# Kernel optimization log

Hardware: AMD Instinct MI355X
Metric: run time of the kernel (lower is better)

Reference implementation:

```python
import jax, jax.numpy as jnp
import numpy as np
from jax import lax

# GlobalSeed with a standard Mamba2 (SSD) core.
# C=64 feature channels, G=8 token dim, d_inner=16, d_state=16, nheads=2, headdim=8, d_conv=3.
C_FEAT, G, D_INNER, D_STATE, NHEADS, HEADDIM, D_CONV = 64, 8, 16, 16, 2, 8, 3
CONV_DIM = D_INNER + 2 * D_STATE  # 48
D_IN_PROJ = 2 * D_INNER + 2 * D_STATE + NHEADS  # 66


def setup_inputs() -> dict:
    key = jax.random.key(0)
    ks = jax.random.split(key, 16)
    B, H, W = 16, 128, 128
    s = 0.02
    return {
        "x": jax.random.normal(ks[0], (B, C_FEAT, H, W), jnp.float32),
        "tok_w": s * jax.random.normal(ks[1], (G, C_FEAT), jnp.float32),
        "tok_b": jnp.zeros((G,), jnp.float32),
        "detok_w": s * jax.random.normal(ks[2], (C_FEAT, G), jnp.float32),
        "detok_b": jnp.zeros((C_FEAT,), jnp.float32),
        "in_proj_w": s * jax.random.normal(ks[3], (D_IN_PROJ, G), jnp.float32),
        "in_proj_b": jnp.zeros((D_IN_PROJ,), jnp.float32),
        "conv_w": s * jax.random.normal(ks[4], (CONV_DIM, D_CONV), jnp.float32),
        "conv_b": jnp.zeros((CONV_DIM,), jnp.float32),
        "A_log": jnp.log(jnp.arange(1, NHEADS + 1, dtype=jnp.float32)),
        "D": jnp.ones((NHEADS,), jnp.float32),
        "dt_bias": 0.1 * jax.random.normal(ks[5], (NHEADS,), jnp.float32),
        "norm_w": jnp.ones((D_INNER,), jnp.float32),
        "out_w": s * jax.random.normal(ks[6], (G, D_INNER), jnp.float32),
        "out_b": jnp.zeros((G,), jnp.float32),
    }


def _mamba2(gt, in_proj_w, in_proj_b, conv_w, conv_b, A_log, D, dt_bias, norm_w, out_w, out_b):
    # gt: (B, L, G) tokens
    B, L, _ = gt.shape
    zxbcdt = gt @ in_proj_w.T + in_proj_b  # (B, L, 66)
    z = zxbcdt[..., :D_INNER]
    xBC = zxbcdt[..., D_INNER:D_INNER + CONV_DIM]
    dt = zxbcdt[..., D_INNER + CONV_DIM:]  # (B, L, nheads)
    # depthwise causal conv1d over L
    xBC = lax.conv_general_dilated(
        xBC.transpose(0, 2, 1), conv_w[:, None, :], (1,), [(D_CONV - 1, 0)],
        feature_group_count=CONV_DIM).transpose(0, 2, 1) + conv_b
    xBC = jax.nn.silu(xBC)
    xr = xBC[..., :D_INNER].reshape(B, L, NHEADS, HEADDIM)
    Bm = xBC[..., D_INNER:D_INNER + D_STATE]   # (B, L, N)
    Cm = xBC[..., D_INNER + D_STATE:]          # (B, L, N)
    dt = jax.nn.softplus(dt + dt_bias)          # (B, L, H)
    dec = jnp.exp(dt * (-jnp.exp(A_log)))       # (B, L, H)

    def step(h, inp):
        xt, Bt, Ct, dtt, dct = inp  # (B,H,P) (B,N) (B,N) (B,H) (B,H)
        h = dct[:, :, None, None] * h + (dtt[:, :, None] * xt)[..., None] * Bt[:, None, None, :]
        y = jnp.einsum('bhpn,bn->bhp', h, Ct)
        return h, y

    h0 = jnp.zeros((B, NHEADS, HEADDIM, D_STATE), gt.dtype)
    xs = (xr.transpose(1, 0, 2, 3), Bm.transpose(1, 0, 2), Cm.transpose(1, 0, 2),
          dt.transpose(1, 0, 2), dec.transpose(1, 0, 2))
    _, ys = lax.scan(step, h0, xs)  # (L, B, H, P)
    y = ys.transpose(1, 0, 2, 3) + D[None, None, :, None] * xr
    y = y.reshape(B, L, D_INNER)
    y = y * jax.nn.silu(z)  # gated
    y = y * lax.rsqrt(jnp.mean(y * y, axis=-1, keepdims=True) + 1e-5) * norm_w  # RMSNormGated
    return y @ out_w.T + out_b  # (B, L, G)


def reference(x, tok_w, tok_b, detok_w, detok_b, in_proj_w, in_proj_b, conv_w, conv_b,
              A_log, D, dt_bias, norm_w, out_w, out_b):
    B, C, H, W = x.shape
    L = H * W
    g = jnp.einsum('bchw,gc->bghw', x, tok_w) + tok_b[None, :, None, None]
    gt = g.reshape(B, G, L).transpose(0, 2, 1)  # (B, L, G)
    gt = _mamba2(gt, in_proj_w, in_proj_b, conv_w, conv_b, A_log, D, dt_bias, norm_w, out_w, out_b) + gt
    g2 = gt.transpose(0, 2, 1).reshape(B, G, H, W)
    return x + jnp.einsum('bghw,cg->bchw', g2, detok_w) + detok_b[None, :, None, None]
```

## Files before the change

kernel.cpp:

```cpp
#include <hip/hip_runtime.h>
#include <math.h>

#define NB 16
#define CF 64
#define LL 16384
#define GG 8
#define NH 2
#define CHN 64
#define NCH 256
#define NGRP 16

static constexpr size_t OFF_GT = 0;
static constexpr size_t OFF_C  = OFF_GT + (size_t)NB*LL*GG;
static constexpr size_t OFF_YL = OFF_C  + (size_t)NB*LL*16;
static constexpr size_t OFF_CA = OFF_YL + (size_t)NB*LL*16;
static constexpr size_t OFF_U2 = OFF_CA + (size_t)NB*LL*NH;
static constexpr size_t OFF_AC = OFF_U2 + (size_t)NB*NCH*256;
static constexpr size_t OFF_PH = OFF_AC + (size_t)NB*NCH*NH;
static constexpr size_t OFF_CP = OFF_PH + (size_t)NB*NCH*256;
static constexpr size_t OFF_UG = OFF_CP + (size_t)NB*NCH*NH;
static constexpr size_t OFF_AG = OFF_UG + (size_t)NB*NGRP*256;
static constexpr size_t OFF_GH = OFF_AG + (size_t)NB*NGRP*NH;
static constexpr size_t OFF_G2 = OFF_GH + (size_t)NB*NGRP*256;
static constexpr size_t WS_FLOATS = OFF_G2 + (size_t)NB*LL*GG;

typedef float f32x4 __attribute__((ext_vector_type(4)));
typedef short bf16x8 __attribute__((ext_vector_type(8)));

__device__ __forceinline__ float siluf(float v){ return v / (1.f + __expf(-v)); }
__device__ __forceinline__ float softplusf(float v){ return v > 20.f ? v : log1pf(__expf(v)); }

__device__ __forceinline__ unsigned short f2bf(float f){
    unsigned int u = __float_as_uint(f);
    u += 0x7fffu + ((u >> 16) & 1u);
    return (unsigned short)(u >> 16);
}
__device__ __forceinline__ float bf2f(unsigned short s){
    return __uint_as_float(((unsigned int)s) << 16);
}

__device__ __forceinline__ void load8(float* d, const float* p){
    float4 a = ((const float4*)p)[0];
    float4 b = ((const float4*)p)[1];
    d[0]=a.x; d[1]=a.y; d[2]=a.z; d[3]=a.w;
    d[4]=b.x; d[5]=b.y; d[6]=b.z; d[7]=b.w;
}
__device__ __forceinline__ void load16(float* d, const float* p){
    load8(d, p); load8(d+8, p+8);
}

__global__ __launch_bounds__(64) void k1a_tok(
    const float* __restrict__ x, const float* __restrict__ tok_w,
    const float* __restrict__ tok_b, float* __restrict__ gtw)
{
    __shared__ float s_tok[GG*CF];
    int tid = threadIdx.x;
    int b  = blockIdx.x >> 6;
    int ck = blockIdx.x & 63;
    int l0 = (ck << 8) + (tid << 2);
    for (int i = tid; i < GG*CF; i += 64) s_tok[i] = tok_w[i];
    __syncthreads();
    float acc[4][GG];
    #pragma unroll
    for (int r = 0; r < 4; ++r)
        #pragma unroll
        for (int g = 0; g < GG; ++g) acc[r][g] = tok_b[g];
    const float* xb = x + (size_t)b*CF*LL + l0;
    #pragma unroll 8
    for (int c = 0; c < CF; ++c) {
        float4 xv = *(const float4*)(xb + (size_t)c*LL);
        float xa[4] = {xv.x, xv.y, xv.z, xv.w};
        #pragma unroll
        for (int g = 0; g < GG; ++g) {
            float w = s_tok[g*CF + c];
            #pragma unroll
            for (int r = 0; r < 4; ++r) acc[r][g] = fmaf(xa[r], w, acc[r][g]);
        }
    }
    float* gp = gtw + ((size_t)b*LL + l0)*GG;
    #pragma unroll
    for (int r = 0; r < 4; ++r) {
        ((float4*)gp)[r*2+0] = make_float4(acc[r][0],acc[r][1],acc[r][2],acc[r][3]);
        ((float4*)gp)[r*2+1] = make_float4(acc[r][4],acc[r][5],acc[r][6],acc[r][7]);
    }
}

__global__ __launch_bounds__(256, 3) void k2_ssd(
    const float* __restrict__ gtw,
    const float* __restrict__ ipw, const float* __restrict__ ipb,
    const float* __restrict__ cw, const float* __restrict__ cb,
    const float* __restrict__ A_log, const float* __restrict__ dt_bias,
    const float* __restrict__ Dv,
    float* __restrict__ cmw, float* __restrict__ ylw, float* __restrict__ caw,
    float* __restrict__ U2w, float* __restrict__ Acw)
{
    __shared__ __align__(16) unsigned short Cbf[64*40];
    __shared__ __align__(16) unsigned short Bbf[64*40];
    __shared__ __align__(16) unsigned short XTbf[16*72];
    __shared__ __align__(16) unsigned short BTbf[16*72];
    __shared__ __align__(16) unsigned short WXbf[16*72];
    __shared__ __align__(16) unsigned short M0[64*72];
    __shared__ __align__(16) unsigned short M1[64*72];
    __shared__ __align__(16) float s_xf[64*20];
    __shared__ float s_dt[64][2], s_nda[64][2], s_la[64][2], s_w[64][2];
    __shared__ float s_ipw[48*8], s_ipb2[48], s_cw2[144], s_cb2[48], s_wdt[16];

    int tid = threadIdx.x;
    int b = blockIdx.x >> 8, c = blockIdx.x & 255;
    for (int i = tid; i < 384; i += 256) s_ipw[i] = ipw[128 + i];
    if (tid < 48) { s_ipb2[tid] = ipb[16 + tid]; s_cb2[tid] = cb[tid]; }
    else if (tid >= 64 && tid < 208) s_cw2[tid - 64] = cw[tid - 64];
    else if (tid >= 224 && tid < 240) s_wdt[tid - 224] = ipw[512 + (tid - 224)];
    __syncthreads();

    float a0e = __expf(A_log[0]), a1e = __expf(A_log[1]);
    float dtb0 = dt_bias[0], dtb1 = dt_bias[1];
    float bdt0 = ipb[64], bdt1 = ipb[65];
    float D0 = Dv[0], D1 = Dv[1];

    {
        int r = tid >> 2, sub = tid & 3;
        int l = c*CHN + r;
        size_t gb = ((size_t)b*LL + l)*GG;
        float g0[8], g1[8], g2v[8];
        #pragma unroll
        for (int g = 0; g < 8; ++g) { g1[g] = 0.f; g2v[g] = 0.f; }
        load8(g0, gtw + gb);
        if (l >= 1) load8(g1, gtw + gb - GG);
        if (l >= 2) load8(g2v, gtw + gb - 2*GG);
        #pragma unroll
        for (int k = 0; k < 12; ++k) {
            int ch = sub*12 + k;
            float bia = s_ipb2[ch];
            float tA = bia, tB = bia, tC = bia;
            #pragma unroll
            for (int g = 0; g < 8; ++g) {
                float wv = s_ipw[ch*8+g];
                tA = fmaf(g0[g],  wv, tA);
                tB = fmaf(g1[g],  wv, tB);
                tC = fmaf(g2v[g], wv, tC);
            }
            if (l < 1) tB = 0.f;
            if (l < 2) tC = 0.f;
            float a = s_cb2[ch];
            a = fmaf(tC, s_cw2[ch*3+0], a);
            a = fmaf(tB, s_cw2[ch*3+1], a);
            a = fmaf(tA, s_cw2[ch*3+2], a);
            float v = siluf(a);
            if (ch < 16) {
                s_xf[r*20 + ch] = v;
                XTbf[ch*72 + r] = f2bf(v);
            } else if (ch < 32) {
                int n = ch - 16;
                unsigned short bv = f2bf(v);
                Bbf[r*40 + n] = bv;
                BTbf[n*72 + r] = bv;
            } else {
                Cbf[r*40 + (ch - 32)] = f2bf(v);
            }
        }
        unsigned int* cz = (unsigned int*)&Cbf[r*40 + 16];
        unsigned int* bz = (unsigned int*)&Bbf[r*40 + 16];
        cz[sub*2+0] = 0u; cz[sub*2+1] = 0u;
        bz[sub*2+0] = 0u; bz[sub*2+1] = 0u;
        if (sub == 0) {
            float d0 = bdt0, d1 = bdt1;
            #pragma unroll
            for (int g = 0; g < 8; ++g) {
                d0 = fmaf(g0[g], s_wdt[g],   d0);
                d1 = fmaf(g0[g], s_wdt[8+g], d1);
            }
            float dt0 = softplusf(d0 + dtb0), dt1 = softplusf(d1 + dtb1);
            s_dt[r][0] = dt0; s_dt[r][1] = dt1;
            s_nda[r][0] = -dt0*a0e; s_nda[r][1] = -dt1*a1e;
        }
    }
    __syncthreads();

    if (tid < 64) {
        int rr = tid;
        float v0 = s_nda[rr][0], v1 = s_nda[rr][1];
        #pragma unroll
        for (int off = 1; off < 64; off <<= 1) {
            float t0 = __shfl_up(v0, off);
            float t1 = __shfl_up(v1, off);
            if (rr >= off) { v0 += t0; v1 += t1; }
        }
        s_la[rr][0] = v0; s_la[rr][1] = v1;
        *(float2*)(caw + ((size_t)b*LL + c*CHN + rr)*2) =
            make_float2(__expf(v0), __expf(v1));
        float f0 = __shfl(v0, 63), f1 = __shfl(v1, 63);
        s_w[rr][0] = __expf(f0 - v0) * s_dt[rr][0];
        s_w[rr][1] = __expf(f1 - v1) * s_dt[rr][1];
        if (rr == 63)
            *(float2*)(Acw + ((size_t)b*NCH + c)*2) = make_float2(__expf(f0), __expf(f1));
    }
    {
        int rr = tid >> 2, q = tid & 3;
        float4 cv;
        cv.x = bf2f(Cbf[rr*40 + q*4 + 0]);
        cv.y = bf2f(Cbf[rr*40 + q*4 + 1]);
        cv.z = bf2f(Cbf[rr*40 + q*4 + 2]);
        cv.w = bf2f(Cbf[rr*40 + q*4 + 3]);
        ((float4*)(cmw + ((size_t)b*LL + c*CHN + rr)*16))[q] = cv;
    }
    __syncthreads();

    int lane = tid & 63, wv = tid >> 6;
    int ar = lane & 15;
    int kb = lane >> 4;
    int trow = wv*16 + kb*4;

    {
        bf16x8 aC = *(const bf16x8*)&Cbf[(wv*16 + ar)*40 + kb*8];
        float lr0 = s_la[wv*16][0], lr1 = s_la[wv*16][1];
        float ef0[4], ef1[4];
        #pragma unroll
        for (int rg = 0; rg < 4; ++rg) {
            ef0[rg] = __expf(s_la[trow+rg][0] - lr0);
            ef1[rg] = __expf(s_la[trow+rg][1] - lr1);
        }
        for (int ss = 0; ss < 4; ++ss) {
            int s = ss*16 + ar;
            if (ss > wv) {
                #pragma unroll
                for (int rg = 0; rg < 4; ++rg) {
                    M0[(trow+rg)*72 + s] = 0;
                    M1[(trow+rg)*72 + s] = 0;
                }
                continue;
            }
            f32x4 g = {0.f, 0.f, 0.f, 0.f};
            bf16x8 bB = *(const bf16x8*)&Bbf[(ss*16 + ar)*40 + kb*8];
            g = __builtin_amdgcn_mfma_f32_16x16x32_bf16(aC, bB, g, 0, 0, 0);
            float ec0 = __expf(lr0 - s_la[s][0]) * s_dt[s][0];
            float ec1 = __expf(lr1 - s_la[s][1]) * s_dt[s][1];
            #pragma unroll
            for (int rg = 0; rg < 4; ++rg) {
                int t = trow + rg;
                float gv = g[rg];
                float m0 = (s <= t) ? ef0[rg]*ec0*gv : 0.f;
                float m1 = (s <= t) ? ef1[rg]*ec1*gv : 0.f;
                M0[t*72 + s] = f2bf(m0);
                M1[t*72 + s] = f2bf(m1);
            }
        }
    }
    #pragma unroll
    for (int i = 0; i < 4; ++i) {
        int e = tid + 256*i;
        int s = e >> 4, pp = e & 15;
        WXbf[pp*72 + s] = f2bf(s_w[s][pp>>3] * s_xf[s*20 + pp]);
    }
    __syncthreads();

    float* yb = (float*)Cbf;
    {
        int p = ar;
        #pragma unroll
        for (int h = 0; h < 2; ++h) {
            const unsigned short* Mh = h ? M1 : M0;
            f32x4 acc = {0.f, 0.f, 0.f, 0.f};
            #pragma unroll
            for (int kk = 0; kk < 2; ++kk) {
                bf16x8 am = *(const bf16x8*)&Mh[(wv*16 + ar)*72 + kk*32 + kb*8];
                bf16x8 bx = {0,0,0,0,0,0,0,0};
                if (p < 8) bx = *(const bf16x8*)&XTbf[(h*8 + p)*72 + kk*32 + kb*8];
                acc = __builtin_amdgcn_mfma_f32_16x16x32_bf16(am, bx, acc, 0, 0, 0);
            }
            if (p < 8) {
                float Dh = h ? D1 : D0;
                #pragma unroll
                for (int rg = 0; rg < 4; ++rg) {
                    int t = trow + rg;
                    yb[t*20 + h*8 + p] = fmaf(Dh, s_xf[t*20 + h*8 + p], acc[rg]);
                }
            }
        }
    }
    if (wv == 0) {
        f32x4 acc = {0.f, 0.f, 0.f, 0.f};
        #pragma unroll
        for (int kk = 0; kk < 2; ++kk) {
            bf16x8 aw = *(const bf16x8*)&WXbf[ar*72 + kk*32 + kb*8];
            bf16x8 bb = *(const bf16x8*)&BTbf[ar*72 + kk*32 + kb*8];
            acc = __builtin_amdgcn_mfma_f32_16x16x32_bf16(aw, bb, acc, 0, 0, 0);
        }
        #pragma unroll
        for (int rg = 0; rg < 4; ++rg) {
            int pr = kb*4 + rg;
            U2w[(((size_t)b*NCH + c) << 8) + pr*16 + ar] = acc[rg];
        }
    }
    __syncthreads();

    {
        int rr = tid >> 2, q = tid & 3;
        ((float4*)(ylw + ((size_t)b*LL + c*CHN + rr)*16))[q] = *(float4*)&yb[rr*20 + q*4];
    }
}

__global__ void k4c1(const float* __restrict__ U2w, const float* __restrict__ Acw,
                     float* __restrict__ phw, float* __restrict__ cpw,
                     float* __restrict__ Ugw, float* __restrict__ Agw)
{
    int b = blockIdx.x >> 4, grp = blockIdx.x & 15;
    int e = threadIdx.x, he = e >> 7;
    size_t base = (size_t)b*NCH + grp*16;
    float u[16], A[16];
    #pragma unroll
    for (int j = 0; j < 16; ++j) u[j] = U2w[((base + j) << 8) + e];
    #pragma unroll
    for (int j = 0; j < 16; ++j) A[j] = Acw[(base + j)*2 + he];
    float h = 0.f, cp = 1.f;
    #pragma unroll
    for (int j = 0; j < 16; ++j) {
        phw[((base + j) << 8) + e] = h;
        if ((e & 127) == 0) cpw[(base + j)*2 + he] = cp;
        h = fmaf(A[j], h, u[j]);
        cp *= A[j];
    }
    Ugw[(((size_t)b*NGRP + grp) << 8) + e] = h;
    if ((e & 127) == 0) Agw[((size_t)b*NGRP + grp)*2 + he] = cp;
}

__global__ void k4c2(const float* __restrict__ Ugw, const float* __restrict__ Agw,
                     float* __restrict__ ghw)
{
    int b = blockIdx.x, e = threadIdx.x, he = e >> 7;
    float u[NGRP], ag[NGRP];
    #pragma unroll
    for (int g = 0; g < NGRP; ++g) {
        u[g]  = Ugw[(((size_t)b*NGRP + g) << 8) + e];
        ag[g] = Agw[((size_t)b*NGRP + g)*2 + he];
    }
    float h = 0.f;
    #pragma unroll
    for (int g = 0; g < NGRP; ++g) {
        ghw[(((size_t)b*NGRP + g) << 8) + e] = h;
        h = fmaf(ag[g], h, u[g]);
    }
}

__global__ __launch_bounds__(256, 4) void k5a_epi(
    const float* __restrict__ gtw, const float* __restrict__ cmw,
    const float* __restrict__ ylw, const float* __restrict__ caw,
    const float* __restrict__ phw, const float* __restrict__ cpw,
    const float* __restrict__ ghw,
    const float* __restrict__ ipw, const float* __restrict__ ipb,
    const float* __restrict__ norm_w,
    const float* __restrict__ out_w, const float* __restrict__ out_b,
    float* __restrict__ g2w)
{
    __shared__ float s_hin[4][256];
    __shared__ float s_zw[16*GG], s_ow[GG*16];
    int tid = threadIdx.x;
    int b  = blockIdx.x >> 6;
    int ck = blockIdx.x & 63;
    int grpg = ck >> 2;
    float gh = ghw[(((size_t)b*NGRP + grpg) << 8) + tid];
    #pragma unroll
    for (int k = 0; k < 4; ++k) {
        int chn = ck*4 + k;
        float cpv = cpw[((size_t)b*NCH + chn)*2 + (tid >> 7)];
        s_hin[k][tid] = fmaf(cpv, gh, phw[(((size_t)b*NCH + chn) << 8) + tid]);
    }
    if (tid < 128) s_zw[tid] = ipw[tid];
    else s_ow[tid-128] = out_w[tid-128];
    __syncthreads();
    size_t pb = (size_t)b*LL + (ck<<8) + tid;
    int sub = tid >> 6;
    float gv[8]; load8(gv, gtw + pb*GG);
    float Cv[16], ylv[16];
    load16(Cv,  cmw + pb*16);
    load16(ylv, ylw + pb*16);
    float2 ca = *(const float2*)(caw + pb*2);
    float vv[16], ss = 0.f;
    #pragma unroll
    for (int hp = 0; hp < 16; ++hp) {
        float dot = 0.f;
        #pragma unroll
        for (int nn = 0; nn < 16; ++nn)
            dot = fmaf(Cv[nn], s_hin[sub][(hp>>3)*128 + (hp&7)*16 + nn], dot);
        float zz = ipb[hp];
        #pragma unroll
        for (int g = 0; g < GG; ++g) zz = fmaf(gv[g], s_zw[hp*GG+g], zz);
        float y = fmaf((hp>>3) ? ca.y : ca.x, dot, ylv[hp]);
        float w = y * siluf(zz);
        vv[hp] = w; ss = fmaf(w, w, ss);
    }
    float rn = rsqrtf(ss*(1.f/16.f) + 1e-5f);
    float o[8];
    #pragma unroll
    for (int g = 0; g < GG; ++g) o[g] = out_b[g] + gv[g];
    #pragma unroll
    for (int hp = 0; hp < 16; ++hp) {
        float wv = vv[hp] * rn * norm_w[hp];
        #pragma unroll
        for (int g = 0; g < GG; ++g) o[g] = fmaf(wv, s_ow[g*16+hp], o[g]);
    }
    float* gp = g2w + pb*GG;
    ((float4*)gp)[0] = make_float4(o[0],o[1],o[2],o[3]);
    ((float4*)gp)[1] = make_float4(o[4],o[5],o[6],o[7]);
}

__global__ __launch_bounds__(64) void k5b_detok(
    const float* __restrict__ x, const float* __restrict__ g2w,
    const float* __restrict__ dkw, const float* __restrict__ dkb,
    float* __restrict__ outp)
{
    __shared__ float s_dw[CF*GG];
    __shared__ float s_db[CF];
    int tid = threadIdx.x;
    int b  = blockIdx.x >> 6;
    int ck = blockIdx.x & 63;
    int l0 = (ck << 8) + (tid << 2);
    for (int i = tid; i < CF*GG; i += 64) s_dw[i] = dkw[i];
    s_db[tid] = dkb[tid];
    __syncthreads();
    float g2v[4][8];
    const float* gp = g2w + ((size_t)b*LL + l0)*GG;
    #pragma unroll
    for (int r = 0; r < 4; ++r) load8(g2v[r], gp + r*GG);
    const float* xb = x + (size_t)b*CF*LL + l0;
    float* ob = outp + (size_t)b*CF*LL + l0;
    #pragma unroll 4
    for (int c = 0; c < CF; ++c) {
        float4 xv = *(const float4*)(xb + (size_t)c*LL);
        float bias = s_db[c];
        float oa[4] = {xv.x+bias, xv.y+bias, xv.z+bias, xv.w+bias};
        #pragma unroll
        for (int g = 0; g < GG; ++g) {
            float w = s_dw[c*GG+g];
            #pragma unroll
            for (int r = 0; r < 4; ++r) oa[r] = fmaf(g2v[r][g], w, oa[r]);
        }
        *(float4*)(ob + (size_t)c*LL) = make_float4(oa[0],oa[1],oa[2],oa[3]);
    }
}

extern "C" void kernel_launch(void* const* d_in, const int* in_sizes, int n_in,
                              void* d_out, int out_size, void* d_ws, size_t ws_size,
                              hipStream_t stream) {
    const float* x       = (const float*)d_in[0];
    const float* tok_w   = (const float*)d_in[1];
    const float* tok_b   = (const float*)d_in[2];
    const float* detok_w = (const float*)d_in[3];
    const float* detok_b = (const float*)d_in[4];
    const float* ipw     = (const float*)d_in[5];
    const float* ipb     = (const float*)d_in[6];
    const float* cw      = (const float*)d_in[7];
    const float* cb      = (const float*)d_in[8];
    const float* A_log   = (const float*)d_in[9];
    const float* Dv      = (const float*)d_in[10];
    const float* dt_bias = (const float*)d_in[11];
    const float* norm_w  = (const float*)d_in[12];
    const float* out_w   = (const float*)d_in[13];
    const float* out_b   = (const float*)d_in[14];
    float* ws = (float*)d_ws;
    float* outp = (float*)d_out;

    if (ws_size < WS_FLOATS * sizeof(float)) return;

    k1a_tok<<<NB*64, 64, 0, stream>>>(x, tok_w, tok_b, ws+OFF_GT);
    k2_ssd<<<NB*NCH, 256, 0, stream>>>(ws+OFF_GT, ipw, ipb, cw, cb,
        A_log, dt_bias, Dv, ws+OFF_C, ws+OFF_YL, ws+OFF_CA, ws+OFF_U2, ws+OFF_AC);
    k4c1<<<NB*NGRP, 256, 0, stream>>>(ws+OFF_U2, ws+OFF_AC,
        ws+OFF_PH, ws+OFF_CP, ws+OFF_UG, ws+OFF_AG);
    k4c2<<<NB, 256, 0, stream>>>(ws+OFF_UG, ws+OFF_AG, ws+OFF_GH);
    k5a_epi<<<NB*64, 256, 0, stream>>>(ws+OFF_GT, ws+OFF_C, ws+OFF_YL, ws+OFF_CA,
        ws+OFF_PH, ws+OFF_CP, ws+OFF_GH, ipw, ipb, norm_w, out_w, out_b, ws+OFF_G2);
    k5b_detok<<<NB*64, 64, 0, stream>>>(x, ws+OFF_G2, detok_w, detok_b, outp);
}
```

Before: 129.8 us.

## Split SSD into state-only pass and recompute-fused intra-chunk plus epilogue kernel

The first SSD pass now computes only the chunk-end state contributions (x and B channels). The intra-chunk output, the inter-chunk state correction (done as an extra MFMA with decay-scaled C) and the gated RMSNorm/out-proj epilogue are fused into a second per-chunk kernel that recomputes the conv/projections. This removes the C, y_local and cumulative-decay intermediates written to and re-read from global memory. In exchange the in_proj/conv/scan work is done twice, and the cross-chunk state term now goes through bf16 MFMA instead of fp32 FMAs.

```diff
diff --git a/kernel.cpp b/kernel.cpp
--- a/kernel.cpp
+++ b/kernel.cpp
@@ -11,10 +11,7 @@
 #define NGRP 16
 
 static constexpr size_t OFF_GT = 0;
-static constexpr size_t OFF_C  = OFF_GT + (size_t)NB*LL*GG;
-static constexpr size_t OFF_YL = OFF_C  + (size_t)NB*LL*16;
-static constexpr size_t OFF_CA = OFF_YL + (size_t)NB*LL*16;
-static constexpr size_t OFF_U2 = OFF_CA + (size_t)NB*LL*NH;
+static constexpr size_t OFF_U2 = OFF_GT + (size_t)NB*LL*GG;
 static constexpr size_t OFF_AC = OFF_U2 + (size_t)NB*NCH*256;
 static constexpr size_t OFF_PH = OFF_AC + (size_t)NB*NCH*NH;
 static constexpr size_t OFF_CP = OFF_PH + (size_t)NB*NCH*256;
@@ -38,15 +35,15 @@
 __device__ __forceinline__ float bf2f(unsigned short s){
     return __uint_as_float(((unsigned int)s) << 16);
 }
+__device__ __forceinline__ unsigned int pack2bf(float lo, float hi){
+    return (unsigned int)f2bf(lo) | ((unsigned int)f2bf(hi) << 16);
+}
 
 __device__ __forceinline__ void load8(float* d, const float* p){
     float4 a = ((const float4*)p)[0];
     float4 b = ((const float4*)p)[1];
     d[0]=a.x; d[1]=a.y; d[2]=a.z; d[3]=a.w;
     d[4]=b.x; d[5]=b.y; d[6]=b.z; d[7]=b.w;
-}
-__device__ __forceinline__ void load16(float* d, const float* p){
-    load8(d, p); load8(d+8, p+8);
 }
 
 __global__ __launch_bounds__(64) void k1a_tok(
@@ -85,38 +82,30 @@
     }
 }
 
-__global__ __launch_bounds__(256, 3) void k2_ssd(
+__global__ __launch_bounds__(256) void k2a_state(
     const float* __restrict__ gtw,
     const float* __restrict__ ipw, const float* __restrict__ ipb,
     const float* __restrict__ cw, const float* __restrict__ cb,
     const float* __restrict__ A_log, const float* __restrict__ dt_bias,
-    const float* __restrict__ Dv,
-    float* __restrict__ cmw, float* __restrict__ ylw, float* __restrict__ caw,
     float* __restrict__ U2w, float* __restrict__ Acw)
 {
-    __shared__ __align__(16) unsigned short Cbf[64*40];
-    __shared__ __align__(16) unsigned short Bbf[64*40];
     __shared__ __align__(16) unsigned short XTbf[16*72];
     __shared__ __align__(16) unsigned short BTbf[16*72];
     __shared__ __align__(16) unsigned short WXbf[16*72];
-    __shared__ __align__(16) unsigned short M0[64*72];
-    __shared__ __align__(16) unsigned short M1[64*72];
-    __shared__ __align__(16) float s_xf[64*20];
-    __shared__ float s_dt[64][2], s_nda[64][2], s_la[64][2], s_w[64][2];
-    __shared__ float s_ipw[48*8], s_ipb2[48], s_cw2[144], s_cb2[48], s_wdt[16];
+    __shared__ float s_dt[64][2], s_nda[64][2];
+    __shared__ float s_ipw[256], s_ipb2[32], s_cw2[96], s_cb2[32], s_wdt[16];
 
     int tid = threadIdx.x;
     int b = blockIdx.x >> 8, c = blockIdx.x & 255;
-    for (int i = tid; i < 384; i += 256) s_ipw[i] = ipw[128 + i];
-    if (tid < 48) { s_ipb2[tid] = ipb[16 + tid]; s_cb2[tid] = cb[tid]; }
-    else if (tid >= 64 && tid < 208) s_cw2[tid - 64] = cw[tid - 64];
+    s_ipw[tid] = ipw[128 + tid];
+    if (tid < 32) { s_ipb2[tid] = ipb[16 + tid]; s_cb2[tid] = cb[tid]; }
+    else if (tid >= 64 && tid < 160) s_cw2[tid - 64] = cw[tid - 64];
     else if (tid >= 224 && tid < 240) s_wdt[tid - 224] = ipw[512 + (tid - 224)];
     __syncthreads();
 
     float a0e = __expf(A_log[0]), a1e = __expf(A_log[1]);
     float dtb0 = dt_bias[0], dtb1 = dt_bias[1];
     float bdt0 = ipb[64], bdt1 = ipb[65];
-    float D0 = Dv[0], D1 = Dv[1];
 
     {
         int r = tid >> 2, sub = tid & 3;
@@ -129,8 +118,8 @@
         if (l >= 1) load8(g1, gtw + gb - GG);
         if (l >= 2) load8(g2v, gtw + gb - 2*GG);
         #pragma unroll
-        for (int k = 0; k < 12; ++k) {
-            int ch = sub*12 + k;
+        for (int k = 0; k < 8; ++k) {
+            int ch = sub*8 + k;
             float bia = s_ipb2[ch];
             float tA = bia, tB = bia, tC = bia;
             #pragma unroll
@@ -147,22 +136,9 @@
             a = fmaf(tB, s_cw2[ch*3+1], a);
             a = fmaf(tA, s_cw2[ch*3+2], a);
             float v = siluf(a);
-            if (ch < 16) {
-                s_xf[r*20 + ch] = v;
-                XTbf[ch*72 + r] = f2bf(v);
-            } else if (ch < 32) {
-                int n = ch - 16;
-                unsigned short bv = f2bf(v);
-                Bbf[r*40 + n] = bv;
-                BTbf[n*72 + r] = bv;
-            } else {
-                Cbf[r*40 + (ch - 32)] = f2bf(v);
-            }
-        }
-        unsigned int* cz = (unsigned int*)&Cbf[r*40 + 16];
-        unsigned int* bz = (unsigned int*)&Bbf[r*40 + 16];
-        cz[sub*2+0] = 0u; cz[sub*2+1] = 0u;
-        bz[sub*2+0] = 0u; bz[sub*2+1] = 0u;
+            if (ch < 16) XTbf[ch*72 + r] = f2bf(v);
+            else         BTbf[(ch-16)*72 + r] = f2bf(v);
+        }
         if (sub == 0) {
             float d0 = bdt0, d1 = bdt1;
             #pragma unroll
@@ -186,99 +162,17 @@
             float t1 = __shfl_up(v1, off);
             if (rr >= off) { v0 += t0; v1 += t1; }
         }
-        s_la[rr][0] = v0; s_la[rr][1] = v1;
-        *(float2*)(caw + ((size_t)b*LL + c*CHN + rr)*2) =
-            make_float2(__expf(v0), __expf(v1));
         float f0 = __shfl(v0, 63), f1 = __shfl(v1, 63);
-        s_w[rr][0] = __expf(f0 - v0) * s_dt[rr][0];
-        s_w[rr][1] = __expf(f1 - v1) * s_dt[rr][1];
+        float w0 = __expf(f0 - v0) * s_dt[rr][0];
+        float w1 = __expf(f1 - v1) * s_dt[rr][1];
         if (rr == 63)
             *(float2*)(Acw + ((size_t)b*NCH + c)*2) = make_float2(__expf(f0), __expf(f1));
-    }
-    {
-        int rr = tid >> 2, q = tid & 3;
-        float4 cv;
-        cv.x = bf2f(Cbf[rr*40 + q*4 + 0]);
-        cv.y = bf2f(Cbf[rr*40 + q*4 + 1]);
-        cv.z = bf2f(Cbf[rr*40 + q*4 + 2]);
-        cv.w = bf2f(Cbf[rr*40 + q*4 + 3]);
-        ((float4*)(cmw + ((size_t)b*LL + c*CHN + rr)*16))[q] = cv;
-    }
-    __syncthreads();
-
-    int lane = tid & 63, wv = tid >> 6;
-    int ar = lane & 15;
-    int kb = lane >> 4;
-    int trow = wv*16 + kb*4;
-
-    {
-        bf16x8 aC = *(const bf16x8*)&Cbf[(wv*16 + ar)*40 + kb*8];
-        float lr0 = s_la[wv*16][0], lr1 = s_la[wv*16][1];
-        float ef0[4], ef1[4];
-        #pragma unroll
-        for (int rg = 0; rg < 4; ++rg) {
-            ef0[rg] = __expf(s_la[trow+rg][0] - lr0);
-            ef1[rg] = __expf(s_la[trow+rg][1] - lr1);
-        }
-        for (int ss = 0; ss < 4; ++ss) {
-            int s = ss*16 + ar;
-            if (ss > wv) {
-                #pragma unroll
-                for (int rg = 0; rg < 4; ++rg) {
-                    M0[(trow+rg)*72 + s] = 0;
-                    M1[(trow+rg)*72 + s] = 0;
-                }
-                continue;
-            }
-            f32x4 g = {0.f, 0.f, 0.f, 0.f};
-            bf16x8 bB = *(const bf16x8*)&Bbf[(ss*16 + ar)*40 + kb*8];
-            g = __builtin_amdgcn_mfma_f32_16x16x32_bf16(aC, bB, g, 0, 0, 0);
-            float ec0 = __expf(lr0 - s_la[s][0]) * s_dt[s][0];
-            float ec1 = __expf(lr1 - s_la[s][1]) * s_dt[s][1];
-            #pragma unroll
-            for (int rg = 0; rg < 4; ++rg) {
-                int t = trow + rg;
-                float gv = g[rg];
-                float m0 = (s <= t) ? ef0[rg]*ec0*gv : 0.f;
-                float m1 = (s <= t) ? ef1[rg]*ec1*gv : 0.f;
-                M0[t*72 + s] = f2bf(m0);
-                M1[t*72 + s] = f2bf(m1);
-            }
-        }
-    }
-    #pragma unroll
-    for (int i = 0; i < 4; ++i) {
-        int e = tid + 256*i;
-        int s = e >> 4, pp = e & 15;
-        WXbf[pp*72 + s] = f2bf(s_w[s][pp>>3] * s_xf[s*20 + pp]);
-    }
-    __syncthreads();
-
-    float* yb = (float*)Cbf;
-    {
-        int p = ar;
-        #pragma unroll
-        for (int h = 0; h < 2; ++h) {
-            const unsigned short* Mh = h ? M1 : M0;
-            f32x4 acc = {0.f, 0.f, 0.f, 0.f};
-            #pragma unroll
-            for (int kk = 0; kk < 2; ++kk) {
-                bf16x8 am = *(const bf16x8*)&Mh[(wv*16 + ar)*72 + kk*32 + kb*8];
-                bf16x8 bx = {0,0,0,0,0,0,0,0};
-                if (p < 8) bx = *(const bf16x8*)&XTbf[(h*8 + p)*72 + kk*32 + kb*8];
-                acc = __builtin_amdgcn_mfma_f32_16x16x32_bf16(am, bx, acc, 0, 0, 0);
-            }
-            if (p < 8) {
-                float Dh = h ? D1 : D0;
-                #pragma unroll
-                for (int rg = 0; rg < 4; ++rg) {
-                    int t = trow + rg;
-                    yb[t*20 + h*8 + p] = fmaf(Dh, s_xf[t*20 + h*8 + p], acc[rg]);
-                }
-            }
-        }
-    }
-    if (wv == 0) {
+        #pragma unroll
+        for (int pp = 0; pp < 16; ++pp) {
+            float wh = (pp < 8) ? w0 : w1;
+            WXbf[pp*72 + rr] = f2bf(wh * bf2f(XTbf[pp*72 + rr]));
+        }
+        int ar = tid & 15, kb = tid >> 4;
         f32x4 acc = {0.f, 0.f, 0.f, 0.f};
         #pragma unroll
         for (int kk = 0; kk < 2; ++kk) {
@@ -287,16 +181,8 @@
             acc = __builtin_amdgcn_mfma_f32_16x16x32_bf16(aw, bb, acc, 0, 0, 0);
         }
         #pragma unroll
-        for (int rg = 0; rg < 4; ++rg) {
-            int pr = kb*4 + rg;
-            U2w[(((size_t)b*NCH + c) << 8) + pr*16 + ar] = acc[rg];
-        }
-    }
-    __syncthreads();
-
-    {
-        int rr = tid >> 2, q = tid & 3;
-        ((float4*)(ylw + ((size_t)b*LL + c*CHN + rr)*16))[q] = *(float4*)&yb[rr*20 + q*4];
+        for (int rg = 0; rg < 4; ++rg)
+            U2w[(((size_t)b*NCH + c) << 8) + (kb*4+rg)*16 + ar] = acc[rg];
     }
 }
 
@@ -342,66 +228,289 @@
     }
 }
 
-__global__ __launch_bounds__(256, 4) void k5a_epi(
-    const float* __restrict__ gtw, const float* __restrict__ cmw,
-    const float* __restrict__ ylw, const float* __restrict__ caw,
+__global__ __launch_bounds__(256) void k2b_fused(
+    const float* __restrict__ gtw,
+    const float* __restrict__ ipw, const float* __restrict__ ipb,
+    const float* __restrict__ cw, const float* __restrict__ cb,
+    const float* __restrict__ A_log, const float* __restrict__ dt_bias,
+    const float* __restrict__ Dv, const float* __restrict__ norm_w,
+    const float* __restrict__ out_w, const float* __restrict__ out_b,
     const float* __restrict__ phw, const float* __restrict__ cpw,
     const float* __restrict__ ghw,
-    const float* __restrict__ ipw, const float* __restrict__ ipb,
-    const float* __restrict__ norm_w,
-    const float* __restrict__ out_w, const float* __restrict__ out_b,
     float* __restrict__ g2w)
 {
-    __shared__ float s_hin[4][256];
-    __shared__ float s_zw[16*GG], s_ow[GG*16];
+    __shared__ __align__(16) unsigned short Cbf[64*40];
+    __shared__ __align__(16) unsigned short Bbf[64*40];
+    __shared__ __align__(16) unsigned short XTbf[16*72];
+    __shared__ __align__(16) unsigned short Mbf[64*72];
+    __shared__ __align__(16) unsigned short Cp0[64*16];
+    __shared__ __align__(16) unsigned short Cp1[64*16];
+    __shared__ float s_hin[256];
+    __shared__ float s_dt[64][2], s_nda[64][2], s_la[64][2];
+    __shared__ float s_ipw[384], s_ipb2[48], s_cw2[144], s_cb2[48], s_wdt[16];
+    __shared__ float s_zw[128], s_ow[128];
+
     int tid = threadIdx.x;
-    int b  = blockIdx.x >> 6;
-    int ck = blockIdx.x & 63;
-    int grpg = ck >> 2;
-    float gh = ghw[(((size_t)b*NGRP + grpg) << 8) + tid];
-    #pragma unroll
-    for (int k = 0; k < 4; ++k) {
-        int chn = ck*4 + k;
-        float cpv = cpw[((size_t)b*NCH + chn)*2 + (tid >> 7)];
-        s_hin[k][tid] = fmaf(cpv, gh, phw[(((size_t)b*NCH + chn) << 8) + tid]);
-    }
+    int b = blockIdx.x >> 8, c = blockIdx.x & 255;
+
+    {
+        int grp = c >> 4;
+        float gh  = ghw[(((size_t)b*NGRP + grp) << 8) + tid];
+        float cpv = cpw[((size_t)b*NCH + c)*2 + (tid >> 7)];
+        float phv = phw[(((size_t)b*NCH + c) << 8) + tid];
+        s_hin[tid] = fmaf(cpv, gh, phv);
+    }
+    for (int i = tid; i < 384; i += 256) s_ipw[i] = ipw[128 + i];
     if (tid < 128) s_zw[tid] = ipw[tid];
     else s_ow[tid-128] = out_w[tid-128];
-    __syncthreads();
-    size_t pb = (size_t)b*LL + (ck<<8) + tid;
-    int sub = tid >> 6;
-    float gv[8]; load8(gv, gtw + pb*GG);
-    float Cv[16], ylv[16];
-    load16(Cv,  cmw + pb*16);
-    load16(ylv, ylw + pb*16);
-    float2 ca = *(const float2*)(caw + pb*2);
-    float vv[16], ss = 0.f;
-    #pragma unroll
-    for (int hp = 0; hp < 16; ++hp) {
-        float dot = 0.f;
-        #pragma unroll
-        for (int nn = 0; nn < 16; ++nn)
-            dot = fmaf(Cv[nn], s_hin[sub][(hp>>3)*128 + (hp&7)*16 + nn], dot);
-        float zz = ipb[hp];
-        #pragma unroll
-        for (int g = 0; g < GG; ++g) zz = fmaf(gv[g], s_zw[hp*GG+g], zz);
-        float y = fmaf((hp>>3) ? ca.y : ca.x, dot, ylv[hp]);
-        float w = y * siluf(zz);
-        vv[hp] = w; ss = fmaf(w, w, ss);
-    }
-    float rn = rsqrtf(ss*(1.f/16.f) + 1e-5f);
-    float o[8];
-    #pragma unroll
-    for (int g = 0; g < GG; ++g) o[g] = out_b[g] + gv[g];
-    #pragma unroll
-    for (int hp = 0; hp < 16; ++hp) {
-        float wv = vv[hp] * rn * norm_w[hp];
-        #pragma unroll
-        for (int g = 0; g < GG; ++g) o[g] = fmaf(wv, s_ow[g*16+hp], o[g]);
-    }
-    float* gp = g2w + pb*GG;
-    ((float4*)gp)[0] = make_float4(o[0],o[1],o[2],o[3]);
-    ((float4*)gp)[1] = make_float4(o[4],o[5],o[6],o[7]);
+    if (tid < 48) { s_ipb2[tid] = ipb[16 + tid]; s_cb2[tid] = cb[tid]; }
+    else if (tid >= 64 && tid < 208) s_cw2[tid - 64] = cw[tid - 64];
+    else if (tid >= 224 && tid < 240) s_wdt[tid - 224] = ipw[512 + (tid - 224)];
+    __syncthreads();
+
+    float a0e = __expf(A_log[0]), a1e = __expf(A_log[1]);
+    float dtb0 = dt_bias[0], dtb1 = dt_bias[1];
+    float bdt0 = ipb[64], bdt1 = ipb[65];
+    float D0 = Dv[0], D1 = Dv[1];
+
+    {
+        int r = tid >> 2, sub = tid & 3;
+        int l = c*CHN + r;
+        size_t gb = ((size_t)b*LL + l)*GG;
+        float g0[8], g1[8], g2v[8];
+        #pragma unroll
+        for (int g = 0; g < 8; ++g) { g1[g] = 0.f; g2v[g] = 0.f; }
+        load8(g0, gtw + gb);
+        if (l >= 1) load8(g1, gtw + gb - GG);
+        if (l >= 2) load8(g2v, gtw + gb - 2*GG);
+        #pragma unroll
+        for (int k = 0; k < 12; ++k) {
+            int ch = sub*12 + k;
+            float bia = s_ipb2[ch];
+            float tA = bia, tB = bia, tC = bia;
+            #pragma unroll
+            for (int g = 0; g < 8; ++g) {
+                float wv = s_ipw[ch*8+g];
+                tA = fmaf(g0[g],  wv, tA);
+                tB = fmaf(g1[g],  wv, tB);
+                tC = fmaf(g2v[g], wv, tC);
+            }
+            if (l < 1) tB = 0.f;
+            if (l < 2) tC = 0.f;
+            float a = s_cb2[ch];
+            a = fmaf(tC, s_cw2[ch*3+0], a);
+            a = fmaf(tB, s_cw2[ch*3+1], a);
+            a = fmaf(tA, s_cw2[ch*3+2], a);
+            float v = siluf(a);
+            if (ch < 16)      XTbf[ch*72 + r] = f2bf(v);
+            else if (ch < 32) Bbf[r*40 + (ch-16)] = f2bf(v);
+            else              Cbf[r*40 + (ch-32)] = f2bf(v);
+        }
+        unsigned int* cz = (unsigned int*)&Cbf[r*40 + 16];
+        unsigned int* bz = (unsigned int*)&Bbf[r*40 + 16];
+        cz[sub*2+0] = 0u; cz[sub*2+1] = 0u;
+        bz[sub*2+0] = 0u; bz[sub*2+1] = 0u;
+        if (sub == 0) {
+            float d0 = bdt0, d1 = bdt1;
+            #pragma unroll
+            for (int g = 0; g < 8; ++g) {
+                d0 = fmaf(g0[g], s_wdt[g],   d0);
+                d1 = fmaf(g0[g], s_wdt[8+g], d1);
+            }
+            float dt0 = softplusf(d0 + dtb0), dt1 = softplusf(d1 + dtb1);
+            s_dt[r][0] = dt0; s_dt[r][1] = dt1;
+            s_nda[r][0] = -dt0*a0e; s_nda[r][1] = -dt1*a1e;
+        }
+    }
+    __syncthreads();
+
+    int lane = tid & 63, wv = tid >> 6;
+    int ar = lane & 15, kb = lane >> 4;
+    int trow = wv*16 + kb*4;
+
+    f32x4 gT[4];
+    {
+        bf16x8 aC = *(const bf16x8*)&Cbf[(wv*16 + ar)*40 + kb*8];
+        #pragma unroll
+        for (int ss = 0; ss < 4; ++ss) {
+            f32x4 g = {0.f, 0.f, 0.f, 0.f};
+            if (ss <= wv) {
+                bf16x8 bB = *(const bf16x8*)&Bbf[(ss*16 + ar)*40 + kb*8];
+                g = __builtin_amdgcn_mfma_f32_16x16x32_bf16(aC, bB, g, 0, 0, 0);
+            }
+            gT[ss] = g;
+        }
+    }
+    if (tid < 64) {
+        int rr = tid;
+        float v0 = s_nda[rr][0], v1 = s_nda[rr][1];
+        #pragma unroll
+        for (int off = 1; off < 64; off <<= 1) {
+            float t0 = __shfl_up(v0, off);
+            float t1 = __shfl_up(v1, off);
+            if (rr >= off) { v0 += t0; v1 += t1; }
+        }
+        s_la[rr][0] = v0; s_la[rr][1] = v1;
+    }
+    __syncthreads();
+
+    {
+        int h = tid >> 7;
+        int rr = (tid & 127) >> 1;
+        int nh = (tid & 1) * 8;
+        float sc = __expf(s_la[rr][h]);
+        unsigned short* Cp = h ? Cp1 : Cp0;
+        unsigned int* dst = (unsigned int*)&Cp[rr*16 + nh];
+        #pragma unroll
+        for (int j = 0; j < 4; ++j)
+            dst[j] = pack2bf(sc * bf2f(Cbf[rr*40 + nh + j*2]),
+                             sc * bf2f(Cbf[rr*40 + nh + j*2 + 1]));
+    }
+    float lr0 = s_la[wv*16][0], lr1 = s_la[wv*16][1];
+    float ef0[4], ef1[4];
+    #pragma unroll
+    for (int rg = 0; rg < 4; ++rg) {
+        ef0[rg] = __expf(s_la[trow+rg][0] - lr0);
+        ef1[rg] = __expf(s_la[trow+rg][1] - lr1);
+    }
+    {
+        for (int ss = 0; ss < 4; ++ss) {
+            int s = ss*16 + ar;
+            if (ss > wv) {
+                if (!(ar & 1)) {
+                    #pragma unroll
+                    for (int rg = 0; rg < 4; ++rg)
+                        *(unsigned int*)&Mbf[(trow+rg)*72 + ss*16 + ar] = 0u;
+                }
+                continue;
+            }
+            float ec0 = __expf(lr0 - s_la[s][0]) * s_dt[s][0];
+            #pragma unroll
+            for (int rg = 0; rg < 4; ++rg) {
+                float m = (s <= trow+rg) ? ef0[rg]*ec0*gT[ss][rg] : 0.f;
+                float mp = __shfl_xor(m, 1);
+                if (!(ar & 1))
+                    *(unsigned int*)&Mbf[(trow+rg)*72 + ss*16 + ar] = pack2bf(m, mp);
+            }
+        }
+    }
+    __syncthreads();
+
+    f32x4 acc0 = {0.f, 0.f, 0.f, 0.f};
+    {
+        int p = ar;
+        #pragma unroll
+        for (int kk = 0; kk < 2; ++kk) {
+            bf16x8 am = *(const bf16x8*)&Mbf[(wv*16 + ar)*72 + kk*32 + kb*8];
+            bf16x8 bx = {0,0,0,0,0,0,0,0};
+            if (p < 8) bx = *(const bf16x8*)&XTbf[p*72 + kk*32 + kb*8];
+            acc0 = __builtin_amdgcn_mfma_f32_16x16x32_bf16(am, bx, acc0, 0, 0, 0);
+        }
+        bf16x8 aCp = {0,0,0,0,0,0,0,0};
+        if (kb < 2) aCp = *(const bf16x8*)&Cp0[(wv*16 + ar)*16 + kb*8];
+        bf16x8 bh = {0,0,0,0,0,0,0,0};
+        if (kb < 2) {
+            #pragma unroll
+            for (int j = 0; j < 8; ++j)
+                bh[j] = (short)f2bf(s_hin[0*128 + (ar&7)*16 + kb*8 + j]);
+        }
+        acc0 = __builtin_amdgcn_mfma_f32_16x16x32_bf16(aCp, bh, acc0, 0, 0, 0);
+    }
+    __syncthreads();
+
+    {
+        for (int ss = 0; ss < 4; ++ss) {
+            int s = ss*16 + ar;
+            if (ss > wv) {
+                if (!(ar & 1)) {
+                    #pragma unroll
+                    for (int rg = 0; rg < 4; ++rg)
+                        *(unsigned int*)&Mbf[(trow+rg)*72 + ss*16 + ar] = 0u;
+                }
+                continue;
+            }
+            float ec1 = __expf(lr1 - s_la[s][1]) * s_dt[s][1];
+            #pragma unroll
+            for (int rg = 0; rg < 4; ++rg) {
+                float m = (s <= trow+rg) ? ef1[rg]*ec1*gT[ss][rg] : 0.f;
+                float mp = __shfl_xor(m, 1);
+                if (!(ar & 1))
+                    *(unsigned int*)&Mbf[(trow+rg)*72 + ss*16 + ar] = pack2bf(m, mp);
+            }
+        }
+    }
+    __syncthreads();
+
+    float* yb = (float*)Cbf;
+    {
+        int p = ar;
+        f32x4 acc1 = {0.f, 0.f, 0.f, 0.f};
+        #pragma unroll
+        for (int kk = 0; kk < 2; ++kk) {
+            bf16x8 am = *(const bf16x8*)&Mbf[(wv*16 + ar)*72 + kk*32 + kb*8];
+            bf16x8 bx = {0,0,0,0,0,0,0,0};
+            if (p < 8) bx = *(const bf16x8*)&XTbf[(8 + p)*72 + kk*32 + kb*8];
+            acc1 = __builtin_amdgcn_mfma_f32_16x16x32_bf16(am, bx, acc1, 0, 0, 0);
+        }
+        bf16x8 aCp = {0,0,0,0,0,0,0,0};
+        if (kb < 2) aCp = *(const bf16x8*)&Cp1[(wv*16 + ar)*16 + kb*8];
+        bf16x8 bh = {0,0,0,0,0,0,0,0};
+        if (kb < 2) {
+            #pragma unroll
+            for (int j = 0; j < 8; ++j)
+                bh[j] = (short)f2bf(s_hin[1*128 + (ar&7)*16 + kb*8 + j]);
+        }
+        acc1 = __builtin_amdgcn_mfma_f32_16x16x32_bf16(aCp, bh, acc1, 0, 0, 0);
+        if (p < 8) {
+            #pragma unroll
+            for (int rg = 0; rg < 4; ++rg) {
+                int t = trow + rg;
+                yb[t*20 + p]     = fmaf(D0, bf2f(XTbf[p*72 + t]),     acc0[rg]);
+                yb[t*20 + 8 + p] = fmaf(D1, bf2f(XTbf[(8+p)*72 + t]), acc1[rg]);
+            }
+        }
+    }
+    __syncthreads();
+
+    {
+        int r = tid >> 2, q = tid & 3;
+        float gv[8]; load8(gv, gtw + ((size_t)b*LL + c*CHN + r)*GG);
+        float vv[4]; float ssq = 0.f;
+        #pragma unroll
+        for (int j = 0; j < 4; ++j) {
+            int hp = q*4 + j;
+            float zz = ipb[hp];
+            #pragma unroll
+            for (int g = 0; g < 8; ++g) zz = fmaf(gv[g], s_zw[hp*8+g], zz);
+            float y = yb[r*20 + hp];
+            float w = y * siluf(zz);
+            vv[j] = w; ssq = fmaf(w, w, ssq);
+        }
+        ssq += __shfl_xor(ssq, 1);
+        ssq += __shfl_xor(ssq, 2);
+        float rn = rsqrtf(ssq*(1.f/16.f) + 1e-5f);
+        float o[8];
+        #pragma unroll
+        for (int g = 0; g < 8; ++g) o[g] = 0.f;
+        #pragma unroll
+        for (int j = 0; j < 4; ++j) {
+            float wj = vv[j] * rn * norm_w[q*4+j];
+            #pragma unroll
+            for (int g = 0; g < 8; ++g) o[g] = fmaf(wj, s_ow[g*16 + q*4 + j], o[g]);
+        }
+        #pragma unroll
+        for (int g = 0; g < 8; ++g) {
+            o[g] += __shfl_xor(o[g], 1);
+            o[g] += __shfl_xor(o[g], 2);
+        }
+        if (q == 0) {
+            #pragma unroll
+            for (int g = 0; g < 8; ++g) o[g] += out_b[g] + gv[g];
+            float* gp = g2w + ((size_t)b*LL + c*CHN + r)*GG;
+            ((float4*)gp)[0] = make_float4(o[0],o[1],o[2],o[3]);
+            ((float4*)gp)[1] = make_float4(o[4],o[5],o[6],o[7]);
+        }
+    }
 }
 
 __global__ __launch_bounds__(64) void k5b_detok(
@@ -463,12 +572,13 @@
     if (ws_size < WS_FLOATS * sizeof(float)) return;
 
     k1a_tok<<<NB*64, 64, 0, stream>>>(x, tok_w, tok_b, ws+OFF_GT);
-    k2_ssd<<<NB*NCH, 256, 0, stream>>>(ws+OFF_GT, ipw, ipb, cw, cb,
-        A_log, dt_bias, Dv, ws+OFF_C, ws+OFF_YL, ws+OFF_CA, ws+OFF_U2, ws+OFF_AC);
+    k2a_state<<<NB*NCH, 256, 0, stream>>>(ws+OFF_GT, ipw, ipb, cw, cb,
+        A_log, dt_bias, ws+OFF_U2, ws+OFF_AC);
     k4c1<<<NB*NGRP, 256, 0, stream>>>(ws+OFF_U2, ws+OFF_AC,
         ws+OFF_PH, ws+OFF_CP, ws+OFF_UG, ws+OFF_AG);
     k4c2<<<NB, 256, 0, stream>>>(ws+OFF_UG, ws+OFF_AG, ws+OFF_GH);
-    k5a_epi<<<NB*64, 256, 0, stream>>>(ws+OFF_GT, ws+OFF_C, ws+OFF_YL, ws+OFF_CA,
-        ws+OFF_PH, ws+OFF_CP, ws+OFF_GH, ipw, ipb, norm_w, out_w, out_b, ws+OFF_G2);
+    k2b_fused<<<NB*NCH, 256, 0, stream>>>(ws+OFF_GT, ipw, ipb, cw, cb,
+        A_log, dt_bias, Dv, norm_w, out_w, out_b,
+        ws+OFF_PH, ws+OFF_CP, ws+OFF_GH, ws+OFF_G2);
     k5b_detok<<<NB*64, 64, 0, stream>>>(x, ws+OFF_G2, detok_w, detok_b, outp);
 }
```

After: 137.1 us. +5.7%, slower.
